# Kernel tuning notes

Hardware: AMD Instinct MI355X
Metric: run time of the kernel (lower is better)

## Reference

```python
import jax, jax.numpy as jnp
import numpy as np

NUM_GROUPS = 16
EPS = 1e-6


def setup_inputs() -> dict:
    key = jax.random.key(0)
    k1, k2, k3, k4 = jax.random.split(key, 4)
    B, N = 16, 131072
    pred = jax.random.normal(k1, (B, N, 3), dtype=jnp.float32)
    target = jax.random.normal(k2, (B, N, 3), dtype=jnp.float32)
    mask = jax.random.randint(k3, (B, N), 0, 2, dtype=jnp.int32)
    groups = jax.random.randint(k4, (B, N), 0, NUM_GROUPS, dtype=jnp.int32)
    return {"pred": pred, "target": target, "mask": mask, "groups": groups}


def _group_median_normalizer(z, valid, groups):
    """Per-point depth normalizer: lower-median of |z| within each (batch, group)
    over valid points, clamped to EPS; groups with no valid points get 1.0.
    z, valid, groups: (B, N). Returns (B, N)."""
    gids = jnp.arange(NUM_GROUPS, dtype=groups.dtype)
    in_g = (groups[:, None, :] == gids[None, :, None]) & valid[:, None, :]  # (B,G,N)
    inf = jnp.asarray(jnp.inf, z.dtype)
    z_g = jnp.where(in_g, z[:, None, :], inf)        # (B,G,N), invalid -> +inf
    z_sorted = jnp.sort(z_g, axis=-1)                # valid values occupy first cnt slots
    cnt = jnp.sum(in_g, axis=-1)                     # (B,G)
    idx = jnp.maximum(cnt - 1, 0) // 2               # torch lower median index
    med = jnp.take_along_axis(z_sorted, idx[..., None], axis=-1)[..., 0]  # (B,G)
    # empty groups give +inf -> nan_to_num -> 1.0, matching torch's untouched default
    med = jnp.nan_to_num(med, nan=1.0, posinf=1.0, neginf=1.0)
    med_safe = jnp.maximum(jnp.abs(med), EPS)        # clamp(|median|, min=eps)
    return jnp.take_along_axis(med_safe, groups, axis=-1)  # gather per point (B,N)


def _log_transform(x):
    return jnp.sign(x) * jnp.log1p(jnp.abs(x))


def reference(pred, target, mask, groups):
    valid = mask.astype(bool)                        # (B,N)
    # shared depth normalization: denominator from TARGET, used for both
    norm = _group_median_normalizer(target[..., 2], valid, groups)  # (B,N)
    vm = valid[..., None]                            # (B,N,1)
    inv = 1.0 / norm[..., None]
    p = jnp.nan_to_num(jnp.where(vm, pred, 0.0) * inv, nan=0.0, posinf=0.0, neginf=0.0)
    t = jnp.nan_to_num(jnp.where(vm, target, 0.0) * inv, nan=0.0, posinf=0.0, neginf=0.0)
    loss = jnp.abs(_log_transform(p) - _log_transform(t))  # (B,N,3)
    loss = jnp.where(vm, loss, 0.0)
    denom = 3.0 * jnp.sum(valid).astype(jnp.float32) + 1e-6  # expanded mask count
    return jnp.sum(loss) / denom
```

## Files before the change

kernel.cpp:

```cpp
#include <hip/hip_runtime.h>
#include <math.h>

#define NPTS_N 131072
#define NGROUP 16
#define NBG 256
#define CBLK 512
#define BPB 32
#define PPB 4096
#define SEGCAP 256
#define NSEL 6144
#define NACC 64
#define LGRID 1024
#define EPSF 1e-6f

__device__ __forceinline__ unsigned f2key(float f) {
    unsigned u = __float_as_uint(f);
    return (u & 0x80000000u) ? ~u : (u | 0x80000000u);
}
__device__ __forceinline__ float key2f(unsigned k) {
    unsigned u = (k & 0x80000000u) ? (k ^ 0x80000000u) : ~k;
    return __uint_as_float(u);
}
__device__ __forceinline__ float flog1p(float a) {
    return __log2f(1.0f + a) * 0.69314718056f;
}

__global__ __launch_bounds__(256) void compact_kernel(
        const float* __restrict__ target,
        const int* __restrict__ mask,
        const int* __restrict__ groups,
        unsigned* __restrict__ bucket,
        unsigned* __restrict__ blockCnt,
        unsigned char* __restrict__ packed) {
    __shared__ unsigned scnt[NGROUP];
    int tid = threadIdx.x, blk = blockIdx.x;
    int i0 = blk * PPB + tid * 16;
    if (tid < NGROUP) scnt[tid] = 0;
    __syncthreads();
    int4 m[4], g[4];
    #pragma unroll
    for (int k = 0; k < 4; ++k) {
        m[k] = *(const int4*)(mask + i0 + k * 4);
        g[k] = *(const int4*)(groups + i0 + k * 4);
    }
    float f[48];
    const float4* t4 = (const float4*)(target + (size_t)i0 * 3);
    #pragma unroll
    for (int k = 0; k < 12; ++k) *(float4*)(f + 4 * k) = t4[k];
    unsigned pk[4];
    unsigned keys[16]; unsigned meta[16]; unsigned vbits = 0;
    #pragma unroll
    for (int k = 0; k < 4; ++k) {
        int mm[4] = {m[k].x, m[k].y, m[k].z, m[k].w};
        int gg[4] = {g[k].x, g[k].y, g[k].z, g[k].w};
        unsigned pb = 0;
        #pragma unroll
        for (int j = 0; j < 4; ++j) {
            int idx = k * 4 + j;
            unsigned gj = (unsigned)gg[j] & 15u;
            pb |= (gj | (mm[j] ? 0x80u : 0u)) << (8 * j);
            if (mm[j]) {
                keys[idx] = f2key(f[3 * idx + 2]);
                unsigned pos = atomicAdd(&scnt[gj], 1u);
                meta[idx] = (gj << 16) | pos;
                vbits |= 1u << idx;
            }
        }
        pk[k] = pb;
    }
    *(uint4*)(packed + i0) = make_uint4(pk[0], pk[1], pk[2], pk[3]);
    __syncthreads();
    if (tid < NGROUP) blockCnt[blk * NGROUP + tid] = scnt[tid];
    #pragma unroll
    for (int idx = 0; idx < 16; ++idx) {
        if (vbits & (1u << idx)) {
            unsigned gj = meta[idx] >> 16, pos = meta[idx] & 0xFFFFu;
            if (pos < SEGCAP)
                bucket[(size_t)(blk * NGROUP + gj) * SEGCAP + pos] = keys[idx];
        }
    }
}

__global__ __launch_bounds__(1024) void select_kernel(
        const unsigned* __restrict__ bucket,
        const unsigned* __restrict__ blockCnt,
        float* __restrict__ norm,
        unsigned* __restrict__ cnt,
        float* __restrict__ accF,
        unsigned* __restrict__ done) {
    __shared__ unsigned skey[NSEL];
    __shared__ unsigned hist[2048];
    __shared__ unsigned sc[BPB];
    __shared__ unsigned segoff[BPB + 1];
    __shared__ unsigned wsum[16];
    __shared__ unsigned sres[2];
    int bg = blockIdx.x, tid = threadIdx.x;
    int b = bg >> 4, g = bg & 15;
    if (bg == 0) {
        if (tid < NACC) accF[tid] = 0.f;
        if (tid == NACC) *done = 0;
    }
    if (tid < BPB) {
        unsigned s = blockCnt[(b * BPB + tid) * NGROUP + g];
        sc[tid] = s;
        unsigned inc = s;
        #pragma unroll
        for (int o = 1; o < BPB; o <<= 1) {
            unsigned v = __shfl_up(inc, o, 64);
            if (tid >= o) inc += v;
        }
        segoff[tid + 1] = inc;
        if (tid == 0) segoff[0] = 0;
    }
    __syncthreads();
    unsigned ntrue = segoff[BPB];
    unsigned n = ntrue > NSEL ? NSEL : ntrue;
    if (tid == 0) cnt[bg] = ntrue;
    if (n == 0) { if (tid == 0) norm[bg] = 1.0f; return; }
    int wv = tid >> 6, ln = tid & 63;
    for (int c = wv; c < BPB; c += 16) {
        unsigned count = sc[c], o = segoff[c];
        if (count > SEGCAP) count = SEGCAP;
        const unsigned* src = bucket + (size_t)((b * BPB + c) * NGROUP + g) * SEGCAP;
        for (unsigned j = ln; j < count; j += 64)
            if (o + j < NSEL) skey[o + j] = src[j];
    }
    __syncthreads();

    unsigned rank = (n - 1) >> 1;
    unsigned selkey = 0;
    const int shifts[3] = {21, 10, 0};
    const int widths[3] = {11, 11, 10};
    for (int p = 0; p < 3; ++p) {
        int sft = shifts[p], w = widths[p];
        unsigned nb = 1u << w, bmask = nb - 1;
        for (unsigned j = tid; j < nb; j += 1024) hist[j] = 0;
        __syncthreads();
        for (unsigned j = tid; j < n; j += 1024) {
            unsigned key = skey[j];
            bool in = (p == 0) || ((key >> (sft + w)) == selkey);
            if (in) atomicAdd(&hist[(key >> sft) & bmask], 1u);
        }
        __syncthreads();
        unsigned cpl = nb >> 10;
        unsigned basebin = tid * cpl;
        unsigned s = 0;
        for (unsigned j = 0; j < cpl; ++j) s += hist[basebin + j];
        unsigned inc = s;
        #pragma unroll
        for (int o = 1; o < 64; o <<= 1) {
            unsigned v = __shfl_up(inc, o, 64);
            if ((tid & 63) >= o) inc += v;
        }
        if ((tid & 63) == 63) wsum[tid >> 6] = inc;
        __syncthreads();
        unsigned woff = 0;
        for (int w2 = 0; w2 < (tid >> 6); ++w2) woff += wsum[w2];
        unsigned excl = woff + inc - s;
        if (rank >= excl && rank < excl + s) {
            unsigned run = excl, binSel = basebin;
            for (unsigned j = 0; j < cpl; ++j) {
                unsigned h = hist[basebin + j];
                if (run + h > rank) { binSel = basebin + j; break; }
                run += h;
            }
            sres[0] = binSel; sres[1] = rank - run;
        }
        __syncthreads();
        selkey = (selkey << w) | sres[0];
        rank = sres[1];
        __syncthreads();
    }
    if (tid == 0) norm[bg] = fmaxf(fabsf(key2f(selkey)), EPSF);
}

__global__ __launch_bounds__(256) void loss_kernel(
        const float* __restrict__ pred,
        const float* __restrict__ target,
        const unsigned char* __restrict__ packed,
        const float* __restrict__ norm,
        const unsigned* __restrict__ cnt,
        float* __restrict__ accF,
        unsigned* __restrict__ done,
        float* __restrict__ out) {
    __shared__ float sinv[NGROUP];
    __shared__ float swsum[4];
    __shared__ bool isLast;
    __shared__ float red[256];
    __shared__ float accSum;
    int tid = threadIdx.x;
    int blk = blockIdx.x;
    int b = blk >> 6;
    if (tid < NGROUP) sinv[tid] = 1.0f / norm[(b << 4) + tid];
    __syncthreads();
    int p0 = b * NPTS_N + (blk & 63) * 2048 + tid * 8;
    uint2 pkw = *(const uint2*)(packed + p0);
    const float4* pr4 = (const float4*)(pred + (size_t)p0 * 3);
    const float4* tg4 = (const float4*)(target + (size_t)p0 * 3);
    float pv[24], tv[24];
    #pragma unroll
    for (int k = 0; k < 6; ++k) { *(float4*)(pv + 4 * k) = pr4[k]; *(float4*)(tv + 4 * k) = tg4[k]; }
    float acc = 0.f;
    #pragma unroll
    for (int q = 0; q < 8; ++q) {
        unsigned byte = ((q < 4 ? pkw.x : pkw.y) >> (8 * (q & 3))) & 0xFFu;
        if (byte & 0x80u) {
            float inv = sinv[byte & 15u];
            #pragma unroll
            for (int c = 0; c < 3; ++c) {
                float pp = pv[q * 3 + c] * inv;
                float tt = tv[q * 3 + c] * inv;
                float lp = copysignf(flog1p(fabsf(pp)), pp);
                float lt = copysignf(flog1p(fabsf(tt)), tt);
                acc += fabsf(lp - lt);
            }
        }
    }
    #pragma unroll
    for (int off = 32; off; off >>= 1) acc += __shfl_down(acc, off, 64);
    if ((tid & 63) == 0) swsum[tid >> 6] = acc;
    __syncthreads();
    if (tid == 0) {
        float v = swsum[0] + swsum[1] + swsum[2] + swsum[3];
        atomicAdd(&accF[blk & (NACC - 1)], v);
        __asm__ volatile("s_waitcnt vmcnt(0)" ::: "memory");
        unsigned old = __hip_atomic_fetch_add(done, 1u, __ATOMIC_RELAXED,
                                              __HIP_MEMORY_SCOPE_AGENT);
        isLast = (old == (unsigned)(LGRID - 1));
    }
    __syncthreads();
    if (isLast) {
        float s = 0.f;
        if (tid < NACC)
            s = __hip_atomic_load(&accF[tid], __ATOMIC_RELAXED, __HIP_MEMORY_SCOPE_AGENT);
        #pragma unroll
        for (int off = 32; off; off >>= 1) s += __shfl_down(s, off, 64);
        if (tid == 0) accSum = s;
        red[tid] = (float)cnt[tid];
        __syncthreads();
        for (int st = 128; st; st >>= 1) {
            if (tid < st) red[tid] += red[tid + st];
            __syncthreads();
        }
        if (tid == 0) out[0] = accSum / (3.0f * red[0] + 1e-6f);
    }
}

extern "C" void kernel_launch(void* const* d_in, const int* in_sizes, int n_in,
                              void* d_out, int out_size, void* d_ws, size_t ws_size,
                              hipStream_t stream) {
    const float* pred   = (const float*)d_in[0];
    const float* target = (const float*)d_in[1];
    const int*   mask   = (const int*)d_in[2];
    const int*   groups = (const int*)d_in[3];
    float* out = (float*)d_out;

    char* ws = (char*)d_ws;
    const size_t MB = 1024 * 1024;
    unsigned*      bucket   = (unsigned*)ws;
    unsigned char* packed   = (unsigned char*)(ws + 8 * MB);
    unsigned*      blockCnt = (unsigned*)(ws + 10 * MB);
    unsigned*      cnt      = (unsigned*)(ws + 10 * MB + 32768);
    float*         normv    = (float*)(ws + 10 * MB + 32768 + 1024);
    float*         accF     = (float*)(ws + 10 * MB + 32768 + 2048);
    unsigned*      done     = (unsigned*)(ws + 10 * MB + 32768 + 3072);

    compact_kernel<<<dim3(CBLK), dim3(256), 0, stream>>>(target, mask, groups,
                                                         bucket, blockCnt, packed);
    select_kernel<<<dim3(NBG), dim3(1024), 0, stream>>>(bucket, blockCnt, normv, cnt, accF, done);
    loss_kernel<<<dim3(LGRID), dim3(256), 0, stream>>>(pred, target, packed, normv,
                                                       cnt, accF, done, out);
}
```

Measured before the change: 124.3 us.

## Replace three-pass radix select with one histogram pass plus candidate rank counting

The per-(batch,group) median select now runs one 11-bit histogram pass over the top key bits to find the bin holding the median. It then compacts the keys in that bin into a shared candidate buffer and finds the exact rank by brute-force pairwise counting. This removes two histogram passes and their barriers and prefix scans. The pairwise count costs O(m^2) in the candidate count and is capped at 2048 candidates, which is a correctness risk if a bin ever holds more keys.

```diff
diff --git a/kernel.cpp b/kernel.cpp
--- a/kernel.cpp
+++ b/kernel.cpp
@@ -9,6 +9,7 @@
 #define PPB 4096
 #define SEGCAP 256
 #define NSEL 6144
+#define CCAP 2048
 #define NACC 64
 #define LGRID 1024
 #define EPSF 1e-6f
@@ -90,10 +91,12 @@
         unsigned* __restrict__ done) {
     __shared__ unsigned skey[NSEL];
     __shared__ unsigned hist[2048];
+    __shared__ unsigned cand[CCAP];
     __shared__ unsigned sc[BPB];
     __shared__ unsigned segoff[BPB + 1];
     __shared__ unsigned wsum[16];
     __shared__ unsigned sres[2];
+    __shared__ unsigned candn;
     int bg = blockIdx.x, tid = threadIdx.x;
     int b = bg >> 4, g = bg & 15;
     if (bg == 0) {
@@ -112,6 +115,8 @@
         segoff[tid + 1] = inc;
         if (tid == 0) segoff[0] = 0;
     }
+    if (tid == 0) candn = 0;
+    hist[tid] = 0; if (tid < 1024) hist[tid + 1024] = 0;
     __syncthreads();
     unsigned ntrue = segoff[BPB];
     unsigned n = ntrue > NSEL ? NSEL : ntrue;
@@ -128,50 +133,49 @@
     __syncthreads();
 
     unsigned rank = (n - 1) >> 1;
-    unsigned selkey = 0;
-    const int shifts[3] = {21, 10, 0};
-    const int widths[3] = {11, 11, 10};
-    for (int p = 0; p < 3; ++p) {
-        int sft = shifts[p], w = widths[p];
-        unsigned nb = 1u << w, bmask = nb - 1;
-        for (unsigned j = tid; j < nb; j += 1024) hist[j] = 0;
-        __syncthreads();
-        for (unsigned j = tid; j < n; j += 1024) {
-            unsigned key = skey[j];
-            bool in = (p == 0) || ((key >> (sft + w)) == selkey);
-            if (in) atomicAdd(&hist[(key >> sft) & bmask], 1u);
-        }
-        __syncthreads();
-        unsigned cpl = nb >> 10;
-        unsigned basebin = tid * cpl;
-        unsigned s = 0;
-        for (unsigned j = 0; j < cpl; ++j) s += hist[basebin + j];
-        unsigned inc = s;
-        #pragma unroll
-        for (int o = 1; o < 64; o <<= 1) {
-            unsigned v = __shfl_up(inc, o, 64);
-            if ((tid & 63) >= o) inc += v;
-        }
-        if ((tid & 63) == 63) wsum[tid >> 6] = inc;
-        __syncthreads();
-        unsigned woff = 0;
-        for (int w2 = 0; w2 < (tid >> 6); ++w2) woff += wsum[w2];
-        unsigned excl = woff + inc - s;
-        if (rank >= excl && rank < excl + s) {
-            unsigned run = excl, binSel = basebin;
-            for (unsigned j = 0; j < cpl; ++j) {
-                unsigned h = hist[basebin + j];
-                if (run + h > rank) { binSel = basebin + j; break; }
-                run += h;
-            }
-            sres[0] = binSel; sres[1] = rank - run;
-        }
-        __syncthreads();
-        selkey = (selkey << w) | sres[0];
-        rank = sres[1];
-        __syncthreads();
-    }
-    if (tid == 0) norm[bg] = fmaxf(fabsf(key2f(selkey)), EPSF);
+    for (unsigned j = tid; j < n; j += 1024)
+        atomicAdd(&hist[skey[j] >> 21], 1u);
+    __syncthreads();
+    unsigned basebin = tid * 2;
+    unsigned s = hist[basebin] + hist[basebin + 1];
+    unsigned inc = s;
+    #pragma unroll
+    for (int o = 1; o < 64; o <<= 1) {
+        unsigned v = __shfl_up(inc, o, 64);
+        if ((tid & 63) >= o) inc += v;
+    }
+    if ((tid & 63) == 63) wsum[tid >> 6] = inc;
+    __syncthreads();
+    unsigned woff = 0;
+    for (int w2 = 0; w2 < (tid >> 6); ++w2) woff += wsum[w2];
+    unsigned excl = woff + inc - s;
+    if (rank >= excl && rank < excl + s) {
+        unsigned h0 = hist[basebin];
+        if (excl + h0 > rank) { sres[0] = basebin;     sres[1] = rank - excl; }
+        else                  { sres[0] = basebin + 1; sres[1] = rank - excl - h0; }
+    }
+    __syncthreads();
+    const unsigned binSel = sres[0], rr = sres[1];
+    for (unsigned j = tid; j < n; j += 1024) {
+        unsigned key = skey[j];
+        if ((key >> 21) == binSel) {
+            unsigned p = atomicAdd(&candn, 1u);
+            if (p < CCAP) cand[p] = key;
+        }
+    }
+    __syncthreads();
+    unsigned m2 = candn; if (m2 > CCAP) m2 = CCAP;
+    for (unsigned j = tid; j < m2; j += 1024) {
+        unsigned kj = cand[j];
+        unsigned cl = 0, ce = 0;
+        for (unsigned i = 0; i < m2; ++i) {
+            unsigned ki = cand[i];
+            cl += (ki < kj) ? 1u : 0u;
+            ce += (ki == kj) ? 1u : 0u;
+        }
+        if (cl <= rr && rr < cl + ce)
+            norm[bg] = fmaxf(fabsf(key2f(kj)), EPSF);
+    }
 }
 
 __global__ __launch_bounds__(256) void loss_kernel(
```

Result: no change. 124.1 us (-0.1%).
